# Kernel tuning notes

Measured on AMD Instinct MI355X. Metric: run time of the kernel, lower is better.

## Reference

```python
import jax, jax.numpy as jnp
import numpy as np

E = 1024
H = 16
D = E // H
S = 2048
B = 2

def setup_inputs() -> dict:
    key = jax.random.key(0)
    ks = jax.random.split(key, 5)
    x = jax.random.normal(ks[0], (B, S, E), dtype=jnp.float32)
    W_qkv = jax.random.normal(ks[1], (E, 3 * E), dtype=jnp.float32) / np.sqrt(E)
    b_qkv = jax.random.normal(ks[2], (3 * E,), dtype=jnp.float32) * 0.02
    W_out = jax.random.normal(ks[3], (E, E), dtype=jnp.float32) / np.sqrt(E)
    b_out = jax.random.normal(ks[4], (E,), dtype=jnp.float32) * 0.02
    return {"x": x, "W_qkv": W_qkv, "b_qkv": b_qkv, "W_out": W_out, "b_out": b_out}

def reference(x, W_qkv, b_qkv, W_out, b_out):
    b, s, e = x.shape
    qkv = x @ W_qkv + b_qkv                      # [B,S,3E]
    q, k, v = jnp.split(qkv, 3, axis=-1)
    # [B,S,E] -> [B,H,S,D]
    q = q.reshape(b, s, H, D).transpose(0, 2, 1, 3)
    k = k.reshape(b, s, H, D).transpose(0, 2, 1, 3)
    v = v.reshape(b, s, H, D).transpose(0, 2, 1, 3)
    scale = 1.0 / np.sqrt(D)
    att = jnp.einsum('bhqd,bhkd->bhqk', q, k) * scale
    causal = jnp.tril(jnp.ones((s, s), dtype=bool))
    att = jnp.where(causal[None, None], att, -jnp.inf)
    att = jax.nn.softmax(att, axis=-1)
    out = jnp.einsum('bhqk,bhkd->bhqd', att, v)  # [B,H,S,D]
    out = out.transpose(0, 2, 1, 3).reshape(b, s, e)
    return out @ W_out + b_out
```

## Files before the change

### kernel.cpp

```cpp
#include <hip/hip_runtime.h>

typedef unsigned short u16;
typedef __bf16  bf16x8 __attribute__((ext_vector_type(8)));
typedef float   f32x4  __attribute__((ext_vector_type(4)));
typedef unsigned int   u32x4 __attribute__((ext_vector_type(4)));
typedef unsigned short u16x4 __attribute__((ext_vector_type(4)));

#define BB 2
#define HH 16
#define DD 64
#define SS 2048
#define EE 1024

#define BM 128
#define BN 128

#define QSCALE 0.1803368801111244f

static __device__ __forceinline__ u16 f2bf(float f) {
    unsigned int u = __float_as_uint(f);
    u += 0x7FFFu + ((u >> 16) & 1u);
    return (u16)(u >> 16);
}

union BfCast { u32x4 u; bf16x8 b; };
static __device__ __forceinline__ bf16x8 ldb8(const u16* p) {
    BfCast x; x.u = *(const u32x4*)p; return x.b;
}

static __device__ __forceinline__ void gload16(const u16* g, u16* l) {
    __builtin_amdgcn_global_load_lds(
        (const __attribute__((address_space(1))) unsigned int*)g,
        (__attribute__((address_space(3))) unsigned int*)l, 16, 0, 0);
}

static __device__ __forceinline__ int kidx(int s, int d) {
    return (((s >> 4) * 2 + (d >> 5)) * 512) + ((((d >> 3) & 3) * 16 + (s & 15)) * 8) + (d & 7);
}
static __device__ __forceinline__ int vidx(int key, int d) {
    return (((key >> 5) * 4 + (d >> 4)) * 512) + ((((key >> 3) & 3) * 16 + (d & 15)) * 8) + (key & 7);
}

__global__ __launch_bounds__(256) void conv_kernel(
    const float* __restrict__ in, u16* __restrict__ out, int n4)
{
    int i = blockIdx.x * blockDim.x + threadIdx.x;
    if (i < n4) {
        f32x4 v = ((const f32x4*)in)[i];
        u16x4 o;
        o[0] = f2bf(v[0]); o[1] = f2bf(v[1]); o[2] = f2bf(v[2]); o[3] = f2bf(v[3]);
        ((u16x4*)out)[i] = o;
    }
}

__global__ __launch_bounds__(256) void transpose_kernel(
    const float* __restrict__ in, u16* __restrict__ out, int R, int C)
{
    __shared__ float tile[32][33];
    const int tx = threadIdx.x & 31;
    const int ty = threadIdx.x >> 5;
    const int ct = C >> 5;
    const int bc = blockIdx.x % ct;
    const int br = blockIdx.x / ct;
    const int c0 = bc * 32, r0 = br * 32;
    #pragma unroll
    for (int i = 0; i < 4; i++)
        tile[ty + i * 8][tx] = in[(r0 + ty + i * 8) * C + c0 + tx];
    __syncthreads();
    #pragma unroll
    for (int i = 0; i < 4; i++)
        out[(c0 + ty + i * 8) * R + r0 + tx] = f2bf(tile[tx][ty + i * 8]);
}

__global__ __launch_bounds__(256) void gemm_qkv_kernel(
    const u16* __restrict__ A,
    const u16* __restrict__ BT,
    const float* __restrict__ bias,
    u16* __restrict__ Qb, u16* __restrict__ Kb, u16* __restrict__ Vb)
{
    __shared__ __align__(16) u16 As[2][BM * 32];
    __shared__ __align__(16) u16 Bs[2][BN * 32];
    const int K = EE;
    const int lane = threadIdx.x & 63;
    const int wave = threadIdx.x >> 6;
    const int nb = 3 * EE / BN;
    const int tm = blockIdx.x / nb, tn = blockIdx.x % nb;
    const int lm = lane & 15, quad = lane >> 4;

    const int srow = wave * 32 + (lane >> 2);
    const int scol = (lane & 3) * 8;
    const u16* ag = A  + (tm * BM + srow) * K + scol;
    const u16* bg = BT + (tn * BN + srow) * K + scol;
    const int lofs = wave * 1024;

    const int wy = wave >> 1, wx = wave & 1;
    f32x4 acc[4][4] = {};

    gload16(ag,          &As[0][lofs]);
    gload16(ag + 16 * K, &As[0][lofs + 512]);
    gload16(bg,          &Bs[0][lofs]);
    gload16(bg + 16 * K, &Bs[0][lofs + 512]);
    ag += 32; bg += 32;

    for (int it = 0; it < 32; ++it) {
        const int cur = it & 1;
        __syncthreads();
        if (it + 1 < 32) {
            gload16(ag,          &As[cur ^ 1][lofs]);
            gload16(ag + 16 * K, &As[cur ^ 1][lofs + 512]);
            gload16(bg,          &Bs[cur ^ 1][lofs]);
            gload16(bg + 16 * K, &Bs[cur ^ 1][lofs + 512]);
            ag += 32; bg += 32;
        }
        bf16x8 af[4], bf[4];
        #pragma unroll
        for (int i = 0; i < 4; i++) {
            af[i] = ldb8(&As[cur][(wy * 64 + i * 16 + lm) * 32 + quad * 8]);
            bf[i] = ldb8(&Bs[cur][(wx * 64 + i * 16 + lm) * 32 + quad * 8]);
        }
        #pragma unroll
        for (int mi = 0; mi < 4; mi++)
            #pragma unroll
            for (int ni = 0; ni < 4; ni++)
                acc[mi][ni] = __builtin_amdgcn_mfma_f32_16x16x32_bf16(af[mi], bf[ni], acc[mi][ni], 0, 0, 0);
    }

    const int gm0 = tm * BM + wy * 64;
    const int gn0 = tn * BN + wx * 64;
    #pragma unroll
    for (int ni = 0; ni < 4; ni++) {
        const int n = gn0 + ni * 16 + lm;
        const float bv = bias[n];
        const int which = n >> 10;
        const int e = n & 1023;
        const int h = e >> 6, d = e & 63;
        #pragma unroll
        for (int mi = 0; mi < 4; mi++) {
            if (which == 2) {
                const int m0 = gm0 + mi * 16 + quad * 4;
                const int b = m0 >> 11, key0 = m0 & 2047;
                u16x4 pk;
                #pragma unroll
                for (int r = 0; r < 4; r++) pk[r] = f2bf(acc[mi][ni][r] + bv);
                *(u16x4*)&Vb[(b * HH + h) * 131072 + vidx(key0, d)] = pk;
            } else if (which == 1) {
                #pragma unroll
                for (int r = 0; r < 4; r++) {
                    const int m = gm0 + mi * 16 + quad * 4 + r;
                    const int b = m >> 11, s = m & 2047;
                    Kb[(b * HH + h) * 131072 + kidx(s, d)] = f2bf(acc[mi][ni][r] + bv);
                }
            } else {
                #pragma unroll
                for (int r = 0; r < 4; r++) {
                    const int m = gm0 + mi * 16 + quad * 4 + r;
                    const int b = m >> 11, s = m & 2047;
                    Qb[((b * HH + h) * SS + s) * DD + d] = f2bf((acc[mi][ni][r] + bv) * QSCALE);
                }
            }
        }
    }
}

__global__ __launch_bounds__(256) void attn_kernel(
    const u16* __restrict__ Qb, const u16* __restrict__ Kb,
    const u16* __restrict__ Vb, u16* __restrict__ Ob)
{
    __shared__ __align__(16) u16 Ks[2][4096];
    __shared__ __align__(16) u16 Vs[2][4096];
    __shared__ __align__(16) u16 Plds[4 * 16 * 72];
    const int tid = threadIdx.x;
    const int lane = tid & 63, wave = tid >> 6;
    const int lm = lane & 15, quad = lane >> 4;
    const int bh = blockIdx.x & 31;
    const int qt = (SS / 64 - 1) - (blockIdx.x >> 5);
    const int q0 = qt * 64;
    const int qrow = q0 + wave * 16;
    const int b = bh >> 4, h = bh & 15;

    const u16* qbase = Qb + (bh * SS + qrow) * DD;
    const bf16x8 qf0 = ldb8(qbase + lm * DD + quad * 8);
    const bf16x8 qf1 = ldb8(qbase + lm * DD + 32 + quad * 8);

    const u16* ktile = Kb + bh * 131072;
    const u16* vtile = Vb + bh * 131072;
    u16* Pw = Plds + wave * (16 * 72);

    BfCast oc; oc.u = (u32x4){0x3F803F80u, 0x3F803F80u, 0x3F803F80u, 0x3F803F80u};
    const bf16x8 ones = oc.b;

    f32x4 oacc[4] = {};
    f32x4 lacc = {0.f, 0.f, 0.f, 0.f};

    const int ktmax = qt + 1;
    {
        const u16* kg = ktile + wave * 1024 + lane * 8;
        const u16* vg = vtile + wave * 1024 + lane * 8;
        gload16(kg,       &Ks[0][wave * 1024]);
        gload16(kg + 512, &Ks[0][wave * 1024 + 512]);
        gload16(vg,       &Vs[0][wave * 1024]);
        gload16(vg + 512, &Vs[0][wave * 1024 + 512]);
    }
    for (int kt = 0; kt < ktmax; ++kt) {
        const int cur = kt & 1;
        const int k0 = kt * 64;
        __syncthreads();
        if (kt + 1 < ktmax) {
            const u16* kg = ktile + (kt + 1) * 4096 + wave * 1024 + lane * 8;
            const u16* vg = vtile + (kt + 1) * 4096 + wave * 1024 + lane * 8;
            gload16(kg,       &Ks[cur ^ 1][wave * 1024]);
            gload16(kg + 512, &Ks[cur ^ 1][wave * 1024 + 512]);
            gload16(vg,       &Vs[cur ^ 1][wave * 1024]);
            gload16(vg + 512, &Vs[cur ^ 1][wave * 1024 + 512]);
        }

        f32x4 s[4];
        #pragma unroll
        for (int g = 0; g < 4; g++) {
            f32x4 z = {0.f, 0.f, 0.f, 0.f};
            z    = __builtin_amdgcn_mfma_f32_16x16x32_bf16(ldb8(&Ks[cur][(g * 2) * 512 + lane * 8]), qf0, z, 0, 0, 0);
            s[g] = __builtin_amdgcn_mfma_f32_16x16x32_bf16(ldb8(&Ks[cur][(g * 2 + 1) * 512 + lane * 8]), qf1, z, 0, 0, 0);
        }
        if (k0 + 63 > qrow) {
            const int lim = qrow + lm - k0 - quad * 4;
            #pragma unroll
            for (int g = 0; g < 4; g++)
                #pragma unroll
                for (int r = 0; r < 4; r++)
                    if (g * 16 + r > lim) s[g][r] = -INFINITY;
        }
        #pragma unroll
        for (int g = 0; g < 4; g++) {
            u16x4 pk;
            #pragma unroll
            for (int r = 0; r < 4; r++) pk[r] = f2bf(__builtin_amdgcn_exp2f(s[g][r]));
            *(u16x4*)&Pw[lm * 72 + g * 16 + quad * 4] = pk;
        }
        const bf16x8 pf0 = ldb8(&Pw[lm * 72 + quad * 8]);
        const bf16x8 pf1 = ldb8(&Pw[lm * 72 + 32 + quad * 8]);
        lacc = __builtin_amdgcn_mfma_f32_16x16x32_bf16(ones, pf0, lacc, 0, 0, 0);
        lacc = __builtin_amdgcn_mfma_f32_16x16x32_bf16(ones, pf1, lacc, 0, 0, 0);
        #pragma unroll
        for (int dg = 0; dg < 4; dg++) {
            oacc[dg] = __builtin_amdgcn_mfma_f32_16x16x32_bf16(ldb8(&Vs[cur][dg * 512 + lane * 8]), pf0, oacc[dg], 0, 0, 0);
            oacc[dg] = __builtin_amdgcn_mfma_f32_16x16x32_bf16(ldb8(&Vs[cur][(4 + dg) * 512 + lane * 8]), pf1, oacc[dg], 0, 0, 0);
        }
    }
    const float inv = 1.0f / lacc[0];
    u16* obase = Ob + (b * SS + qrow + lm) * EE + h * DD;
    #pragma unroll
    for (int dg = 0; dg < 4; dg++) {
        u16x4 pk;
        #pragma unroll
        for (int r = 0; r < 4; r++) pk[r] = f2bf(oacc[dg][r] * inv);
        *(u16x4*)&obase[dg * 16 + quad * 4] = pk;
    }
}

__global__ __launch_bounds__(256) void gemm_out_kernel(
    const u16* __restrict__ A,
    const u16* __restrict__ BT,
    const float* __restrict__ bias,
    float* __restrict__ Out)
{
    __shared__ __align__(16) u16 As[2][BM * 32];
    __shared__ __align__(16) u16 Bs[2][BN * 32];
    const int K = EE;
    const int lane = threadIdx.x & 63;
    const int wave = threadIdx.x >> 6;
    const int nb = EE / BN;
    const int tm = blockIdx.x / nb, tn = blockIdx.x % nb;
    const int lm = lane & 15, quad = lane >> 4;

    const int srow = wave * 32 + (lane >> 2);
    const int scol = (lane & 3) * 8;
    const u16* ag = A  + (tm * BM + srow) * K + scol;
    const u16* bg = BT + (tn * BN + srow) * K + scol;
    const int lofs = wave * 1024;

    const int wy = wave >> 1, wx = wave & 1;
    f32x4 acc[4][4] = {};

    gload16(ag,          &As[0][lofs]);
    gload16(ag + 16 * K, &As[0][lofs + 512]);
    gload16(bg,          &Bs[0][lofs]);
    gload16(bg + 16 * K, &Bs[0][lofs + 512]);
    ag += 32; bg += 32;

    for (int it = 0; it < 32; ++it) {
        const int cur = it & 1;
        __syncthreads();
        if (it + 1 < 32) {
            gload16(ag,          &As[cur ^ 1][lofs]);
            gload16(ag + 16 * K, &As[cur ^ 1][lofs + 512]);
            gload16(bg,          &Bs[cur ^ 1][lofs]);
            gload16(bg + 16 * K, &Bs[cur ^ 1][lofs + 512]);
            ag += 32; bg += 32;
        }
        bf16x8 af[4], bf[4];
        #pragma unroll
        for (int i = 0; i < 4; i++) {
            af[i] = ldb8(&As[cur][(wy * 64 + i * 16 + lm) * 32 + quad * 8]);
            bf[i] = ldb8(&Bs[cur][(wx * 64 + i * 16 + lm) * 32 + quad * 8]);
        }
        #pragma unroll
        for (int mi = 0; mi < 4; mi++)
            #pragma unroll
            for (int ni = 0; ni < 4; ni++)
                acc[mi][ni] = __builtin_amdgcn_mfma_f32_16x16x32_bf16(af[mi], bf[ni], acc[mi][ni], 0, 0, 0);
    }

    const int gm0 = tm * BM + wy * 64;
    const int gn0 = tn * BN + wx * 64;
    #pragma unroll
    for (int ni = 0; ni < 4; ni++) {
        const int n = gn0 + ni * 16 + lm;
        const float bv = bias[n];
        #pragma unroll
        for (int mi = 0; mi < 4; mi++)
            #pragma unroll
            for (int r = 0; r < 4; r++)
                Out[(gm0 + mi * 16 + quad * 4 + r) * EE + n] = acc[mi][ni][r] + bv;
    }
}

extern "C" void kernel_launch(void* const* d_in, const int* in_sizes, int n_in,
                              void* d_out, int out_size, void* d_ws, size_t ws_size,
                              hipStream_t stream)
{
    const float* x     = (const float*)d_in[0];
    const float* Wqkv  = (const float*)d_in[1];
    const float* bqkv  = (const float*)d_in[2];
    const float* Wout  = (const float*)d_in[3];
    const float* bout  = (const float*)d_in[4];
    float* out = (float*)d_out;

    char* ws = (char*)d_ws;
    u16* xb    = (u16*)(ws + 0);
    u16* wqkvT = (u16*)(ws + 8388608);
    u16* woutT = (u16*)(ws + 14680064);
    u16* Qb    = (u16*)(ws + 16777216);
    u16* Kb    = (u16*)(ws + 25165824);
    u16* Vb    = (u16*)(ws + 33554432);
    u16* Ob    = (u16*)(ws + 41943040);
    if (ws_size < 50331648) return;

    conv_kernel<<<4096, 256, 0, stream>>>(x, xb, (BB * SS * EE) / 4);
    transpose_kernel<<<(EE / 32) * (3 * EE / 32), 256, 0, stream>>>(Wqkv, wqkvT, EE, 3 * EE);
    transpose_kernel<<<(EE / 32) * (EE / 32), 256, 0, stream>>>(Wout, woutT, EE, EE);
    gemm_qkv_kernel<<<(BB * SS / BM) * (3 * EE / BN), 256, 0, stream>>>(xb, wqkvT, bqkv, Qb, Kb, Vb);
    attn_kernel<<<BB * HH * (SS / 64), 256, 0, stream>>>(Qb, Kb, Vb, Ob);
    gemm_out_kernel<<<(BB * SS / BM) * (EE / BN), 256, 0, stream>>>(Ob, woutT, bout, out);
}
```

Baseline: 189.1 us.

## Pre-swizzle GEMM operands into MFMA fragment layout for contiguous loads

The bf16 conversion of x, the weight transposes and the attention output store now write operands in a 16x32 MFMA-fragment-tiled layout. This lets the GEMM kernels fetch each fragment group as one contiguous 1 KB chunk per wave and read LDS with lane-linear addresses. It targets strided global rows and LDS bank conflicts on the fragment reads. The cost is more scattered writes in the producer kernels: the attention epilogue writes 8-byte pieces and the transpose writes 2-byte elements to swizzled addresses.

```diff
diff --git a/kernel.cpp b/kernel.cpp
--- a/kernel.cpp
+++ b/kernel.cpp
@@ -5,6 +5,7 @@
 typedef float   f32x4  __attribute__((ext_vector_type(4)));
 typedef unsigned int   u32x4 __attribute__((ext_vector_type(4)));
 typedef unsigned short u16x4 __attribute__((ext_vector_type(4)));
+typedef unsigned short u16x8 __attribute__((ext_vector_type(8)));
 
 #define BB 2
 #define HH 16
@@ -34,6 +35,9 @@
         (__attribute__((address_space(3))) unsigned int*)l, 16, 0, 0);
 }
 
+static __device__ __forceinline__ int fidx(int m, int k) {
+    return (((m >> 4) * 32 + (k >> 5)) * 512) + ((((k >> 3) & 3) * 16 + (m & 15)) * 8) + (k & 7);
+}
 static __device__ __forceinline__ int kidx(int s, int d) {
     return (((s >> 4) * 2 + (d >> 5)) * 512) + ((((d >> 3) & 3) * 16 + (s & 15)) * 8) + (d & 7);
 }
@@ -41,20 +45,25 @@
     return (((key >> 5) * 4 + (d >> 4)) * 512) + ((((key >> 3) & 3) * 16 + (d & 15)) * 8) + (key & 7);
 }
 
-__global__ __launch_bounds__(256) void conv_kernel(
-    const float* __restrict__ in, u16* __restrict__ out, int n4)
-{
-    int i = blockIdx.x * blockDim.x + threadIdx.x;
-    if (i < n4) {
-        f32x4 v = ((const f32x4*)in)[i];
-        u16x4 o;
-        o[0] = f2bf(v[0]); o[1] = f2bf(v[1]); o[2] = f2bf(v[2]); o[3] = f2bf(v[3]);
-        ((u16x4*)out)[i] = o;
-    }
-}
-
-__global__ __launch_bounds__(256) void transpose_kernel(
-    const float* __restrict__ in, u16* __restrict__ out, int R, int C)
+__global__ __launch_bounds__(256) void conv_frag_kernel(
+    const float* __restrict__ in, u16* __restrict__ out)
+{
+    const int t = blockIdx.x * 256 + threadIdx.x;
+    const int u = t >> 6;
+    const int w = t & 63;
+    const int m = (u >> 5) * 16 + (w & 15);
+    const int k = (u & 31) * 32 + (w >> 4) * 8;
+    const float* p = in + m * 1024 + k;
+    const f32x4 a = *(const f32x4*)p;
+    const f32x4 b = *(const f32x4*)(p + 4);
+    u16x8 o;
+    o[0] = f2bf(a[0]); o[1] = f2bf(a[1]); o[2] = f2bf(a[2]); o[3] = f2bf(a[3]);
+    o[4] = f2bf(b[0]); o[5] = f2bf(b[1]); o[6] = f2bf(b[2]); o[7] = f2bf(b[3]);
+    *(u16x8*)&out[u * 512 + w * 8] = o;
+}
+
+__global__ __launch_bounds__(256) void transpose_frag_kernel(
+    const float* __restrict__ in, u16* __restrict__ out, int C)
 {
     __shared__ float tile[32][33];
     const int tx = threadIdx.x & 31;
@@ -68,55 +77,56 @@
         tile[ty + i * 8][tx] = in[(r0 + ty + i * 8) * C + c0 + tx];
     __syncthreads();
     #pragma unroll
-    for (int i = 0; i < 4; i++)
-        out[(c0 + ty + i * 8) * R + r0 + tx] = f2bf(tile[tx][ty + i * 8]);
+    for (int i = 0; i < 4; i++) {
+        const int n = c0 + ty + i * 8;
+        out[((n >> 4) * 32 + (r0 >> 5)) * 512 + (((tx >> 3) & 3) * 16 + (n & 15)) * 8 + (tx & 7)]
+            = f2bf(tile[tx][ty + i * 8]);
+    }
 }
 
 __global__ __launch_bounds__(256) void gemm_qkv_kernel(
-    const u16* __restrict__ A,
-    const u16* __restrict__ BT,
+    const u16* __restrict__ Af,
+    const u16* __restrict__ Bf,
     const float* __restrict__ bias,
     u16* __restrict__ Qb, u16* __restrict__ Kb, u16* __restrict__ Vb)
 {
     __shared__ __align__(16) u16 As[2][BM * 32];
     __shared__ __align__(16) u16 Bs[2][BN * 32];
-    const int K = EE;
     const int lane = threadIdx.x & 63;
     const int wave = threadIdx.x >> 6;
     const int nb = 3 * EE / BN;
     const int tm = blockIdx.x / nb, tn = blockIdx.x % nb;
     const int lm = lane & 15, quad = lane >> 4;
-
-    const int srow = wave * 32 + (lane >> 2);
-    const int scol = (lane & 3) * 8;
-    const u16* ag = A  + (tm * BM + srow) * K + scol;
-    const u16* bg = BT + (tn * BN + srow) * K + scol;
-    const int lofs = wave * 1024;
+    const int UG = 32 * 512;
+
+    const u16* ag = Af + (tm * 8 + 2 * wave) * UG + lane * 8;
+    const u16* bg = Bf + (tn * 8 + 2 * wave) * UG + lane * 8;
+    const int ld = wave * 1024;
 
     const int wy = wave >> 1, wx = wave & 1;
     f32x4 acc[4][4] = {};
 
-    gload16(ag,          &As[0][lofs]);
-    gload16(ag + 16 * K, &As[0][lofs + 512]);
-    gload16(bg,          &Bs[0][lofs]);
-    gload16(bg + 16 * K, &Bs[0][lofs + 512]);
-    ag += 32; bg += 32;
+    gload16(ag,      &As[0][ld]);
+    gload16(ag + UG, &As[0][ld + 512]);
+    gload16(bg,      &Bs[0][ld]);
+    gload16(bg + UG, &Bs[0][ld + 512]);
+    ag += 512; bg += 512;
 
     for (int it = 0; it < 32; ++it) {
         const int cur = it & 1;
         __syncthreads();
         if (it + 1 < 32) {
-            gload16(ag,          &As[cur ^ 1][lofs]);
-            gload16(ag + 16 * K, &As[cur ^ 1][lofs + 512]);
-            gload16(bg,          &Bs[cur ^ 1][lofs]);
-            gload16(bg + 16 * K, &Bs[cur ^ 1][lofs + 512]);
-            ag += 32; bg += 32;
+            gload16(ag,      &As[cur ^ 1][ld]);
+            gload16(ag + UG, &As[cur ^ 1][ld + 512]);
+            gload16(bg,      &Bs[cur ^ 1][ld]);
+            gload16(bg + UG, &Bs[cur ^ 1][ld + 512]);
+            ag += 512; bg += 512;
         }
         bf16x8 af[4], bf[4];
         #pragma unroll
         for (int i = 0; i < 4; i++) {
-            af[i] = ldb8(&As[cur][(wy * 64 + i * 16 + lm) * 32 + quad * 8]);
-            bf[i] = ldb8(&Bs[cur][(wx * 64 + i * 16 + lm) * 32 + quad * 8]);
+            af[i] = ldb8(&As[cur][(wy * 4 + i) * 512 + lane * 8]);
+            bf[i] = ldb8(&Bs[cur][(wx * 4 + i) * 512 + lane * 8]);
         }
         #pragma unroll
         for (int mi = 0; mi < 4; mi++)
@@ -247,61 +257,59 @@
         }
     }
     const float inv = 1.0f / lacc[0];
-    u16* obase = Ob + (b * SS + qrow + lm) * EE + h * DD;
+    u16* ob = Ob + (((b * SS + qrow) >> 4) * 32 + h * 2) * 512;
     #pragma unroll
     for (int dg = 0; dg < 4; dg++) {
         u16x4 pk;
         #pragma unroll
         for (int r = 0; r < 4; r++) pk[r] = f2bf(oacc[dg][r] * inv);
-        *(u16x4*)&obase[dg * 16 + quad * 4] = pk;
+        *(u16x4*)&ob[(dg >> 1) * 512 + (((dg * 2 + (quad >> 1)) & 3) * 16 + lm) * 8 + (quad & 1) * 4] = pk;
     }
 }
 
 __global__ __launch_bounds__(256) void gemm_out_kernel(
-    const u16* __restrict__ A,
-    const u16* __restrict__ BT,
+    const u16* __restrict__ Af,
+    const u16* __restrict__ Bf,
     const float* __restrict__ bias,
     float* __restrict__ Out)
 {
     __shared__ __align__(16) u16 As[2][BM * 32];
     __shared__ __align__(16) u16 Bs[2][BN * 32];
-    const int K = EE;
     const int lane = threadIdx.x & 63;
     const int wave = threadIdx.x >> 6;
     const int nb = EE / BN;
     const int tm = blockIdx.x / nb, tn = blockIdx.x % nb;
     const int lm = lane & 15, quad = lane >> 4;
-
-    const int srow = wave * 32 + (lane >> 2);
-    const int scol = (lane & 3) * 8;
-    const u16* ag = A  + (tm * BM + srow) * K + scol;
-    const u16* bg = BT + (tn * BN + srow) * K + scol;
-    const int lofs = wave * 1024;
+    const int UG = 32 * 512;
+
+    const u16* ag = Af + (tm * 8 + 2 * wave) * UG + lane * 8;
+    const u16* bg = Bf + (tn * 8 + 2 * wave) * UG + lane * 8;
+    const int ld = wave * 1024;
 
     const int wy = wave >> 1, wx = wave & 1;
     f32x4 acc[4][4] = {};
 
-    gload16(ag,          &As[0][lofs]);
-    gload16(ag + 16 * K, &As[0][lofs + 512]);
-    gload16(bg,          &Bs[0][lofs]);
-    gload16(bg + 16 * K, &Bs[0][lofs + 512]);
-    ag += 32; bg += 32;
+    gload16(ag,      &As[0][ld]);
+    gload16(ag + UG, &As[0][ld + 512]);
+    gload16(bg,      &Bs[0][ld]);
+    gload16(bg + UG, &Bs[0][ld + 512]);
+    ag += 512; bg += 512;
 
     for (int it = 0; it < 32; ++it) {
         const int cur = it & 1;
         __syncthreads();
         if (it + 1 < 32) {
-            gload16(ag,          &As[cur ^ 1][lofs]);
-            gload16(ag + 16 * K, &As[cur ^ 1][lofs + 512]);
-            gload16(bg,          &Bs[cur ^ 1][lofs]);
-            gload16(bg + 16 * K, &Bs[cur ^ 1][lofs + 512]);
-            ag += 32; bg += 32;
+            gload16(ag,      &As[cur ^ 1][ld]);
+            gload16(ag + UG, &As[cur ^ 1][ld + 512]);
+            gload16(bg,      &Bs[cur ^ 1][ld]);
+            gload16(bg + UG, &Bs[cur ^ 1][ld + 512]);
+            ag += 512; bg += 512;
         }
         bf16x8 af[4], bf[4];
         #pragma unroll
         for (int i = 0; i < 4; i++) {
-            af[i] = ldb8(&As[cur][(wy * 64 + i * 16 + lm) * 32 + quad * 8]);
-            bf[i] = ldb8(&Bs[cur][(wx * 64 + i * 16 + lm) * 32 + quad * 8]);
+            af[i] = ldb8(&As[cur][(wy * 4 + i) * 512 + lane * 8]);
+            bf[i] = ldb8(&Bs[cur][(wx * 4 + i) * 512 + lane * 8]);
         }
         #pragma unroll
         for (int mi = 0; mi < 4; mi++)
@@ -345,9 +353,9 @@
     u16* Ob    = (u16*)(ws + 41943040);
     if (ws_size < 50331648) return;
 
-    conv_kernel<<<4096, 256, 0, stream>>>(x, xb, (BB * SS * EE) / 4);
-    transpose_kernel<<<(EE / 32) * (3 * EE / 32), 256, 0, stream>>>(Wqkv, wqkvT, EE, 3 * EE);
-    transpose_kernel<<<(EE / 32) * (EE / 32), 256, 0, stream>>>(Wout, woutT, EE, EE);
+    conv_frag_kernel<<<2048, 256, 0, stream>>>(x, xb);
+    transpose_frag_kernel<<<(EE / 32) * (3 * EE / 32), 256, 0, stream>>>(Wqkv, wqkvT, 3 * EE);
+    transpose_frag_kernel<<<(EE / 32) * (EE / 32), 256, 0, stream>>>(Wout, woutT, EE);
     gemm_qkv_kernel<<<(BB * SS / BM) * (3 * EE / BN), 256, 0, stream>>>(xb, wqkvT, bqkv, Qb, Kb, Vb);
     attn_kernel<<<BB * HH * (SS / 64), 256, 0, stream>>>(Qb, Kb, Vb, Ob);
     gemm_out_kernel<<<(BB * SS / BM) * (EE / BN), 256, 0, stream>>>(Ob, woutT, bout, out);
```

Measured after the change: 185.1 us. 1.02x faster.
